# Kernel optimization log

Hardware: AMD Instinct MI355X
Metric: run time of the kernel (lower is better)

## Reference

```python
import jax, jax.numpy as jnp
import numpy as np

HIDDEN = 1024


def setup_inputs() -> dict:
    key = jax.random.key(0)
    ks = jax.random.split(key, 8)
    B, S, H = 64, 2048, HIDDEN
    scale = 1.0 / np.sqrt(H)
    return {
        "decoder_hidden": jax.random.normal(ks[0], (B, H), jnp.float32),
        "encoder_outputs": jax.random.normal(ks[1], (B, S, 2 * H), jnp.float32),
        "coverage": jax.random.uniform(ks[2], (B, S), jnp.float32),
        "mask": jnp.ones((B, S), jnp.int32),
        # parameters (nn.Linear weight layout: (out, in); we store transposed for x @ W)
        "W_h": jax.random.normal(ks[3], (2 * H, H), jnp.float32) * scale,
        "W_d": jax.random.normal(ks[4], (H, H), jnp.float32) * scale,
        "W_c": jax.random.normal(ks[5], (1, H), jnp.float32) * scale,
        "v": jax.random.normal(ks[6], (H, 1), jnp.float32) * scale,
    }


def reference(decoder_hidden, encoder_outputs, coverage, mask, W_h, W_d, W_c, v):
    # energy: (B, S, H) = tanh(enc@W_h + dec@W_d broadcast over S + coverage*W_c)
    enc_proj = jnp.einsum("bse,eh->bsh", encoder_outputs, W_h)
    dec_proj = (decoder_hidden @ W_d)[:, None, :]            # (B,1,H)
    cov_proj = coverage[:, :, None] * W_c[0][None, None, :]  # (B,S,H)
    energy = jnp.tanh(enc_proj + dec_proj + cov_proj)
    scores = jnp.einsum("bsh,h->bs", energy, v[:, 0])        # (B,S)
    scores = jnp.where(mask == 0, jnp.float32(-10000.0), scores)
    attn_weights = jax.nn.softmax(scores, axis=1)            # (B,S)
    coverage_new = coverage + attn_weights
    context = jnp.einsum("bs,bse->be", attn_weights, encoder_outputs)  # (B,2H)
    return (context, attn_weights, coverage_new)
```

## Files before the change

kernel.cpp:

```cpp
#include <hip/hip_runtime.h>
#include <hip/hip_bf16.h>
#include <stdint.h>

#define BATCH 64
#define SEQ   2048
#define HID   1024
#define EDIM  2048

#define BM 128
#define BN 512
#define BK 32
#define KSTEPS (EDIM / BK)
#define SMEM_BYTES (65536 + 16384 + 512 + 2048)

typedef __bf16 bf16x8 __attribute__((ext_vector_type(8)));
typedef float  f32x16 __attribute__((ext_vector_type(16)));
typedef float  f32x4v __attribute__((ext_vector_type(4)));

__device__ __forceinline__ unsigned short f2bf(float x) {
    __hip_bfloat16 h = __float2bfloat16(x);
    return __builtin_bit_cast(unsigned short, h);
}

__device__ __forceinline__ uint4 pack8(f32x4v f0, f32x4v f1) {
    uint4 r;
    r.x = (unsigned)f2bf(f0.x) | ((unsigned)f2bf(f0.y) << 16);
    r.y = (unsigned)f2bf(f0.z) | ((unsigned)f2bf(f0.w) << 16);
    r.z = (unsigned)f2bf(f1.x) | ((unsigned)f2bf(f1.y) << 16);
    r.w = (unsigned)f2bf(f1.z) | ((unsigned)f2bf(f1.w) << 16);
    return r;
}

__device__ __forceinline__ void gload16(const void* g, void* l) {
    __builtin_amdgcn_global_load_lds(
        (const __attribute__((address_space(1))) void*)g,
        (__attribute__((address_space(3))) void*)l, 16, 0, 0);
}

__device__ __forceinline__ f32x4v ntload4(const float* p) {
    return __builtin_nontemporal_load((const f32x4v*)p);
}

__device__ __forceinline__ int a_addr(int row, int g) {
    return ((row << 6) + (g << 4)) ^ ((row & 7) << 4);
}

__global__ void wh_transpose_kernel(const float* __restrict__ Wh,
                                    unsigned short* __restrict__ Wt) {
    __shared__ float tile[32][33];
    int bx = blockIdx.x & 63;
    int by = blockIdx.x >> 6;
    int e0 = bx * 32, h0 = by * 32;
    int tx = threadIdx.x & 31, ty = threadIdx.x >> 5;
    #pragma unroll
    for (int i = 0; i < 4; ++i)
        tile[ty + 8 * i][tx] = Wh[(size_t)(e0 + ty + 8 * i) * HID + h0 + tx];
    __syncthreads();
    if (ty < 4) {
        uint4 wv;
        unsigned short* ws = (unsigned short*)&wv;
        #pragma unroll
        for (int j = 0; j < 8; ++j) ws[j] = f2bf(tile[ty * 8 + j][tx]);
        int h = h0 + tx;
        *(uint4*)&Wt[(size_t)((e0 >> 3) + ty) * 8192 + (h >> 9) * 4096 + (h & 511) * 8] = wv;
    }
}

__global__ void dec_proj_kernel(const float* __restrict__ dec,
                                const float* __restrict__ Wd,
                                float* __restrict__ dp) {
    int gid = blockIdx.x * 256 + threadIdx.x;
    int b = gid >> 10, h = gid & 1023;
    const float* dr = dec + b * HID;
    float acc = 0.f;
    #pragma unroll 4
    for (int k = 0; k < HID; ++k) acc = fmaf(dr[k], Wd[(size_t)k * HID + h], acc);
    dp[gid] = acc;
}

__global__ __launch_bounds__(512, 2) void scores_kernel(
    const float* __restrict__ enc, const float* __restrict__ cov,
    const unsigned short* __restrict__ Wt, const float* __restrict__ dp,
    const float* __restrict__ Wc, const float* __restrict__ vv,
    float* __restrict__ spart_out)
{
    extern __shared__ char smem[];
    unsigned short* BlS  = (unsigned short*)smem;
    char*  AlB   = smem + 65536;
    float* cov_s = (float*)(smem + 81920);
    float* sred  = (float*)(smem + 82432);

    const int tid  = threadIdx.x;
    const int lane = tid & 63;
    const int wid  = tid >> 6;
    const int wm   = wid >> 2;
    const int wn   = wid & 3;
    const int l31  = lane & 31;
    const int hi   = lane >> 5;

    const int bid  = blockIdx.x;
    const int half = (bid & 7) >> 2;
    const int m    = ((bid >> 3) << 2) | (bid & 3);
    const int b    = m >> 4;
    const int s0   = (m & 15) * BM;

    const float* Abase = enc + (size_t)(b * SEQ + s0) * EDIM;

    const int arow = tid >> 2;
    const int ag   = tid & 3;

    f32x16 acc[2][4];
    #pragma unroll
    for (int mi = 0; mi < 2; ++mi)
        #pragma unroll
        for (int nj = 0; nj < 4; ++nj)
            #pragma unroll
            for (int r = 0; r < 16; ++r) acc[mi][nj][r] = 0.f;

    if (tid < BM) cov_s[tid] = cov[b * SEQ + s0 + tid];

    {
        const unsigned short* bsrc = Wt + half * 4096 + (size_t)tid * 8;
        unsigned short* bdst = BlS + tid * 8;
        #pragma unroll
        for (int j = 0; j < 4; ++j)
            gload16(bsrc + (size_t)j * 8192, bdst + j * 4096);
        const float* ap = Abase + (size_t)arow * EDIM + ag * 8;
        *(uint4*)(AlB + a_addr(arow, ag)) = pack8(ntload4(ap), ntload4(ap + 4));
    }
    __syncthreads();

    f32x4v a0n, a1n;
    for (int kk = 0; kk < KSTEPS; ++kk) {
        const int cur = kk & 1, nxt = cur ^ 1;
        const unsigned short* Bcur = BlS + cur * 16384;
        const char* Acur = AlB + cur * 8192;

        if (kk + 1 < KSTEPS) {
            const unsigned short* bsrc =
                Wt + (size_t)(kk + 1) * 32768 + half * 4096 + (size_t)tid * 8;
            unsigned short* bdst = BlS + nxt * 16384 + tid * 8;
            #pragma unroll
            for (int j = 0; j < 4; ++j)
                gload16(bsrc + (size_t)j * 8192, bdst + j * 4096);
            const float* ap = Abase + (size_t)arow * EDIM + (kk + 1) * BK + ag * 8;
            a0n = ntload4(ap);
            a1n = ntload4(ap + 4);
        }

        #pragma unroll
        for (int ks = 0; ks < 2; ++ks) {
            const int g = 2 * ks + hi;
            bf16x8 afr0 = *(const bf16x8*)(Acur + a_addr(wm * 64 + l31, g));
            bf16x8 afr1 = *(const bf16x8*)(Acur + a_addr(wm * 64 + 32 + l31, g));
            #pragma unroll
            for (int nj = 0; nj < 4; ++nj) {
                bf16x8 bfr = *(const bf16x8*)(Bcur +
                    (size_t)g * 4096 + (size_t)(wn * 128 + nj * 32 + l31) * 8);
                acc[0][nj] = __builtin_amdgcn_mfma_f32_32x32x16_bf16(
                    afr0, bfr, acc[0][nj], 0, 0, 0);
                acc[1][nj] = __builtin_amdgcn_mfma_f32_32x32x16_bf16(
                    afr1, bfr, acc[1][nj], 0, 0, 0);
            }
        }

        if (kk + 1 < KSTEPS)
            *(uint4*)(AlB + nxt * 8192 + a_addr(arow, ag)) = pack8(a0n, a1n);
        __syncthreads();
    }

    float dv[4], wcv[4], vvv[4];
    #pragma unroll
    for (int nj = 0; nj < 4; ++nj) {
        const int h = half * BN + wn * 128 + nj * 32 + l31;
        dv[nj]  = dp[b * HID + h];
        wcv[nj] = Wc[h];
        vvv[nj] = vv[h];
    }
    #pragma unroll
    for (int mi = 0; mi < 2; ++mi) {
        #pragma unroll
        for (int r = 0; r < 16; ++r) {
            const int row = wm * 64 + mi * 32 + (r & 3) + 8 * (r >> 2) + 4 * hi;
            const float cv = cov_s[row];
            float x = 0.f;
            #pragma unroll
            for (int nj = 0; nj < 4; ++nj) {
                float pre = acc[mi][nj][r] + dv[nj] + cv * wcv[nj];
                float pc = fminf(pre, 20.0f);
                float e2 = __expf(2.0f * pc);
                x = fmaf((e2 - 1.0f) / (e2 + 1.0f), vvv[nj], x);
            }
            x += __shfl_xor(x, 1);
            x += __shfl_xor(x, 2);
            x += __shfl_xor(x, 4);
            x += __shfl_xor(x, 8);
            x += __shfl_xor(x, 16);
            if (l31 == 0) sred[row * 4 + wn] = x;
        }
    }
    __syncthreads();
    if (tid < BM) {
        float s = sred[tid * 4] + sred[tid * 4 + 1] + sred[tid * 4 + 2] + sred[tid * 4 + 3];
        spart_out[(size_t)half * BATCH * SEQ + b * SEQ + s0 + tid] = s;
    }
}

__global__ void softmax_kernel(const float* __restrict__ spart,
                               const int* __restrict__ mask,
                               const float* __restrict__ cov,
                               float* __restrict__ out)
{
    __shared__ float red[8];
    int b = blockIdx.x, tid = threadIdx.x;
    float vals[8];
    float mx = -1e30f;
    #pragma unroll
    for (int i = 0; i < 8; ++i) {
        int s = tid + i * 256;
        float sc = spart[b * SEQ + s] + spart[BATCH * SEQ + b * SEQ + s];
        sc = (mask[b * SEQ + s] == 0) ? -10000.0f : sc;
        vals[i] = sc;
        mx = fmaxf(mx, sc);
    }
    for (int m = 1; m < 64; m <<= 1) mx = fmaxf(mx, __shfl_xor(mx, m));
    if ((tid & 63) == 0) red[tid >> 6] = mx;
    __syncthreads();
    mx = fmaxf(fmaxf(red[0], red[1]), fmaxf(red[2], red[3]));
    float sum = 0.f;
    #pragma unroll
    for (int i = 0; i < 8; ++i) { vals[i] = __expf(vals[i] - mx); sum += vals[i]; }
    for (int m = 1; m < 64; m <<= 1) sum += __shfl_xor(sum, m);
    if ((tid & 63) == 0) red[4 + (tid >> 6)] = sum;
    __syncthreads();
    sum = red[4] + red[5] + red[6] + red[7];
    float inv = 1.0f / sum;
    float* attn = out + BATCH * EDIM;
    float* covn = attn + BATCH * SEQ;
    #pragma unroll
    for (int i = 0; i < 8; ++i) {
        int s = tid + i * 256;
        float w = vals[i] * inv;
        attn[b * SEQ + s] = w;
        covn[b * SEQ + s] = cov[b * SEQ + s] + w;
    }
}

__global__ void context_kernel(const float* __restrict__ enc,
                               const float* __restrict__ attn,
                               float* __restrict__ ctx)
{
    __shared__ float w_s[SEQ];
    int b  = blockIdx.x >> 3;
    int e0 = (blockIdx.x & 7) * 256;
    int tid = threadIdx.x;
    for (int i = tid; i < SEQ; i += 256) w_s[i] = attn[b * SEQ + i];
    __syncthreads();
    const float* ep = enc + (size_t)b * SEQ * EDIM + e0 + tid;
    float acc = 0.f;
    #pragma unroll 8
    for (int s = 0; s < SEQ; ++s)
        acc = fmaf(w_s[s], __builtin_nontemporal_load(ep + (size_t)s * EDIM), acc);
    ctx[b * EDIM + e0 + tid] = acc;
}

extern "C" void kernel_launch(void* const* d_in, const int* in_sizes, int n_in,
                              void* d_out, int out_size, void* d_ws, size_t ws_size,
                              hipStream_t stream) {
    const float* dec  = (const float*)d_in[0];
    const float* enc  = (const float*)d_in[1];
    const float* cov  = (const float*)d_in[2];
    const int*   mask = (const int*)d_in[3];
    const float* Wh   = (const float*)d_in[4];
    const float* Wd   = (const float*)d_in[5];
    const float* Wc   = (const float*)d_in[6];
    const float* v    = (const float*)d_in[7];
    float* out = (float*)d_out;

    unsigned short* Wt = (unsigned short*)d_ws;
    float* dp    = (float*)((char*)d_ws + (size_t)HID * EDIM * 2);
    float* spart = dp + BATCH * HID;

    (void)hipFuncSetAttribute((const void*)scores_kernel,
                              hipFuncAttributeMaxDynamicSharedMemorySize, SMEM_BYTES);

    wh_transpose_kernel<<<dim3(64 * 32), dim3(256), 0, stream>>>(Wh, Wt);
    dec_proj_kernel<<<dim3(BATCH * HID / 256), dim3(256), 0, stream>>>(dec, Wd, dp);
    scores_kernel<<<dim3((SEQ * BATCH / BM) * 2), dim3(512), SMEM_BYTES, stream>>>(
        enc, cov, Wt, dp, Wc, v, spart);
    softmax_kernel<<<dim3(BATCH), dim3(256), 0, stream>>>(spart, mask, cov, out);
    context_kernel<<<dim3(BATCH * (EDIM / 256)), dim3(256), 0, stream>>>(enc, out + BATCH * EDIM, out);
}
```

Before: 1.141 ms.

## Deepen scores GEMM pipeline to four-stage LDS ring with prefetch distance two

The scores GEMM main loop moves from a double-buffered B tile with a one-step lookahead to a four-slot LDS ring for B, filled two K-steps ahead, with A held in two register stages. Plain __syncthreads is replaced by explicit s_waitcnt vmcnt/lgkmcnt counts and raw barriers, so only the oldest loads must land before each step. MFMA issue is split into two halves fenced by sched_barrier and raised with s_setprio, so LDS fragment reads overlap the first half of the math. This is meant to hide global-load latency and the stalls at each barrier. In exchange LDS grows to about 150KB per block, and correctness now depends on the hand-written wait counts matching the number of outstanding loads.

```diff
diff --git a/kernel.cpp b/kernel.cpp
--- a/kernel.cpp
+++ b/kernel.cpp
@@ -11,7 +11,7 @@
 #define BN 512
 #define BK 32
 #define KSTEPS (EDIM / BK)
-#define SMEM_BYTES (65536 + 16384 + 512 + 2048)
+#define SMEM_BYTES 150016
 
 typedef __bf16 bf16x8 __attribute__((ext_vector_type(8)));
 typedef float  f32x16 __attribute__((ext_vector_type(16)));
@@ -78,6 +78,8 @@
     dp[gid] = acc;
 }
 
+#define MFMA32(a, bfv, c) __builtin_amdgcn_mfma_f32_32x32x16_bf16(a, bfv, c, 0, 0, 0)
+
 __global__ __launch_bounds__(512, 2) void scores_kernel(
     const float* __restrict__ enc, const float* __restrict__ cov,
     const unsigned short* __restrict__ Wt, const float* __restrict__ dp,
@@ -85,10 +87,10 @@
     float* __restrict__ spart_out)
 {
     extern __shared__ char smem[];
-    unsigned short* BlS  = (unsigned short*)smem;
-    char*  AlB   = smem + 65536;
-    float* cov_s = (float*)(smem + 81920);
-    float* sred  = (float*)(smem + 82432);
+    unsigned short* BlS = (unsigned short*)smem;
+    char*  AlB   = smem + 131072;
+    float* cov_s = (float*)(smem + 147456);
+    float* sred  = (float*)(smem + 147968);
 
     const int tid  = threadIdx.x;
     const int lane = tid & 63;
@@ -105,9 +107,10 @@
     const int s0   = (m & 15) * BM;
 
     const float* Abase = enc + (size_t)(b * SEQ + s0) * EDIM;
-
     const int arow = tid >> 2;
     const int ag   = tid & 3;
+
+    const unsigned short* Bsrc0 = Wt + half * 4096 + (size_t)tid * 8;
 
     f32x16 acc[2][4];
     #pragma unroll
@@ -117,57 +120,87 @@
             #pragma unroll
             for (int r = 0; r < 16; ++r) acc[mi][nj][r] = 0.f;
 
+    f32x4v aL0[2], aL1[2];
+
+    {
+        const float* ap = Abase + (size_t)arow * EDIM + ag * 8;
+        aL0[0] = ntload4(ap); aL1[0] = ntload4(ap + 4);
+    }
+    #pragma unroll
+    for (int j = 0; j < 4; ++j)
+        gload16(Bsrc0 + (size_t)j * 8192, BlS + j * 4096 + tid * 8);
+    asm volatile("s_waitcnt vmcnt(4)" ::: "memory");
+    *(uint4*)(AlB + a_addr(arow, ag)) = pack8(aL0[0], aL1[0]);
+    {
+        const float* ap = Abase + (size_t)arow * EDIM + BK + ag * 8;
+        aL0[1] = ntload4(ap); aL1[1] = ntload4(ap + 4);
+    }
+    #pragma unroll
+    for (int j = 0; j < 4; ++j)
+        gload16(Bsrc0 + (size_t)(4 + j) * 8192, BlS + 16384 + j * 4096 + tid * 8);
+    asm volatile("s_waitcnt vmcnt(6) lgkmcnt(0)" ::: "memory");
+    __builtin_amdgcn_s_barrier();
+
+    for (int kk4 = 0; kk4 < KSTEPS; kk4 += 4) {
+        #pragma unroll
+        for (int u = 0; u < 4; ++u) {
+            const int kk = kk4 + u;
+            if (kk + 2 < KSTEPS) {
+                const float* ap = Abase + (size_t)arow * EDIM + (kk + 2) * BK + ag * 8;
+                aL0[u & 1] = ntload4(ap); aL1[u & 1] = ntload4(ap + 4);
+                const unsigned short* bs = Bsrc0 + (size_t)(kk + 2) * 32768;
+                unsigned short* bd = BlS + ((u + 2) & 3) * 16384 + tid * 8;
+                #pragma unroll
+                for (int j = 0; j < 4; ++j)
+                    gload16(bs + (size_t)j * 8192, bd + j * 4096);
+            }
+            const unsigned short* Bcur = BlS + u * 16384;
+            const char* Acur = AlB + (u & 1) * 8192;
+
+            bf16x8 afr[2][2], bfr[2][4];
+            #pragma unroll
+            for (int ks = 0; ks < 2; ++ks) {
+                const int g = 2 * ks + hi;
+                afr[ks][0] = *(const bf16x8*)(Acur + a_addr(wm * 64 + l31, g));
+                afr[ks][1] = *(const bf16x8*)(Acur + a_addr(wm * 64 + 32 + l31, g));
+                #pragma unroll
+                for (int nj = 0; nj < 4; ++nj)
+                    bfr[ks][nj] = *(const bf16x8*)(Bcur +
+                        (size_t)g * 4096 + (size_t)(wn * 128 + nj * 32 + l31) * 8);
+            }
+            asm volatile("s_waitcnt lgkmcnt(6)" ::: "memory");
+            __builtin_amdgcn_sched_barrier(0);
+            __builtin_amdgcn_s_setprio(1);
+            #pragma unroll
+            for (int nj = 0; nj < 4; ++nj) {
+                acc[0][nj] = MFMA32(afr[0][0], bfr[0][nj], acc[0][nj]);
+                acc[1][nj] = MFMA32(afr[0][1], bfr[0][nj], acc[1][nj]);
+            }
+            __builtin_amdgcn_s_setprio(0);
+            asm volatile("s_waitcnt lgkmcnt(0)" ::: "memory");
+            __builtin_amdgcn_sched_barrier(0);
+            __builtin_amdgcn_s_setprio(1);
+            #pragma unroll
+            for (int nj = 0; nj < 4; ++nj) {
+                acc[0][nj] = MFMA32(afr[1][0], bfr[1][nj], acc[0][nj]);
+                acc[1][nj] = MFMA32(afr[1][1], bfr[1][nj], acc[1][nj]);
+            }
+            __builtin_amdgcn_s_setprio(0);
+
+            if (kk + 1 < KSTEPS)
+                *(uint4*)(AlB + ((u + 1) & 1) * 8192 + a_addr(arow, ag)) =
+                    pack8(aL0[(u + 1) & 1], aL1[(u + 1) & 1]);
+
+            if (kk + 2 < KSTEPS)
+                asm volatile("s_waitcnt vmcnt(6) lgkmcnt(0)" ::: "memory");
+            else
+                asm volatile("s_waitcnt vmcnt(0) lgkmcnt(0)" ::: "memory");
+            __builtin_amdgcn_s_barrier();
+        }
+    }
+
     if (tid < BM) cov_s[tid] = cov[b * SEQ + s0 + tid];
-
-    {
-        const unsigned short* bsrc = Wt + half * 4096 + (size_t)tid * 8;
-        unsigned short* bdst = BlS + tid * 8;
-        #pragma unroll
-        for (int j = 0; j < 4; ++j)
-            gload16(bsrc + (size_t)j * 8192, bdst + j * 4096);
-        const float* ap = Abase + (size_t)arow * EDIM + ag * 8;
-        *(uint4*)(AlB + a_addr(arow, ag)) = pack8(ntload4(ap), ntload4(ap + 4));
-    }
-    __syncthreads();
-
-    f32x4v a0n, a1n;
-    for (int kk = 0; kk < KSTEPS; ++kk) {
-        const int cur = kk & 1, nxt = cur ^ 1;
-        const unsigned short* Bcur = BlS + cur * 16384;
-        const char* Acur = AlB + cur * 8192;
-
-        if (kk + 1 < KSTEPS) {
-            const unsigned short* bsrc =
-                Wt + (size_t)(kk + 1) * 32768 + half * 4096 + (size_t)tid * 8;
-            unsigned short* bdst = BlS + nxt * 16384 + tid * 8;
-            #pragma unroll
-            for (int j = 0; j < 4; ++j)
-                gload16(bsrc + (size_t)j * 8192, bdst + j * 4096);
-            const float* ap = Abase + (size_t)arow * EDIM + (kk + 1) * BK + ag * 8;
-            a0n = ntload4(ap);
-            a1n = ntload4(ap + 4);
-        }
-
-        #pragma unroll
-        for (int ks = 0; ks < 2; ++ks) {
-            const int g = 2 * ks + hi;
-            bf16x8 afr0 = *(const bf16x8*)(Acur + a_addr(wm * 64 + l31, g));
-            bf16x8 afr1 = *(const bf16x8*)(Acur + a_addr(wm * 64 + 32 + l31, g));
-            #pragma unroll
-            for (int nj = 0; nj < 4; ++nj) {
-                bf16x8 bfr = *(const bf16x8*)(Bcur +
-                    (size_t)g * 4096 + (size_t)(wn * 128 + nj * 32 + l31) * 8);
-                acc[0][nj] = __builtin_amdgcn_mfma_f32_32x32x16_bf16(
-                    afr0, bfr, acc[0][nj], 0, 0, 0);
-                acc[1][nj] = __builtin_amdgcn_mfma_f32_32x32x16_bf16(
-                    afr1, bfr, acc[1][nj], 0, 0, 0);
-            }
-        }
-
-        if (kk + 1 < KSTEPS)
-            *(uint4*)(AlB + nxt * 8192 + a_addr(arow, ag)) = pack8(a0n, a1n);
-        __syncthreads();
-    }
+    __syncthreads();
 
     float dv[4], wcv[4], vvv[4];
     #pragma unroll
```

Result: no change. 1.134 ms (-0.6%).

## Shrink score GEMM N-tile to 128 with 256-thread blocks and 8 partial splits

Applied to the files above, without the earlier changes.

Reshapes the scores GEMM tiling. BN drops from 512 to 128 and each block now has 4 waves (256 threads) instead of 8, with static shared memory sized for higher occupancy. The W_h transpose layout changes to match, and the softmax now sums 8 partial score planes instead of 2. Each encoder A tile is now read and converted to bf16 four times as often, since there are 8 N-splits instead of 2, and the nontemporal loads become plain loads. The aim is more resident blocks and better latency hiding, at the cost of much more global traffic on the large encoder tensor.

```diff
diff --git a/kernel.cpp b/kernel.cpp
--- a/kernel.cpp
+++ b/kernel.cpp
@@ -8,10 +8,10 @@
 #define EDIM  2048
 
 #define BM 128
-#define BN 512
+#define BN 128
 #define BK 32
 #define KSTEPS (EDIM / BK)
-#define SMEM_BYTES (65536 + 16384 + 512 + 2048)
+#define BS (BATCH * SEQ)
 
 typedef __bf16 bf16x8 __attribute__((ext_vector_type(8)));
 typedef float  f32x16 __attribute__((ext_vector_type(16)));
@@ -37,10 +37,6 @@
         (__attribute__((address_space(3))) void*)l, 16, 0, 0);
 }
 
-__device__ __forceinline__ f32x4v ntload4(const float* p) {
-    return __builtin_nontemporal_load((const f32x4v*)p);
-}
-
 __device__ __forceinline__ int a_addr(int row, int g) {
     return ((row << 6) + (g << 4)) ^ ((row & 7) << 4);
 }
@@ -62,7 +58,7 @@
         #pragma unroll
         for (int j = 0; j < 8; ++j) ws[j] = f2bf(tile[ty * 8 + j][tx]);
         int h = h0 + tx;
-        *(uint4*)&Wt[(size_t)((e0 >> 3) + ty) * 8192 + (h >> 9) * 4096 + (h & 511) * 8] = wv;
+        *(uint4*)&Wt[(size_t)((e0 >> 3) + ty) * 8192 + (h >> 7) * 1024 + (h & 127) * 8] = wv;
     }
 }
 
@@ -78,101 +74,104 @@
     dp[gid] = acc;
 }
 
-__global__ __launch_bounds__(512, 2) void scores_kernel(
+#define MFMA32(a, bfv, c) __builtin_amdgcn_mfma_f32_32x32x16_bf16(a, bfv, c, 0, 0, 0)
+
+__global__ __launch_bounds__(256, 4) void scores_kernel(
     const float* __restrict__ enc, const float* __restrict__ cov,
     const unsigned short* __restrict__ Wt, const float* __restrict__ dp,
     const float* __restrict__ Wc, const float* __restrict__ vv,
     float* __restrict__ spart_out)
 {
-    extern __shared__ char smem[];
-    unsigned short* BlS  = (unsigned short*)smem;
-    char*  AlB   = smem + 65536;
-    float* cov_s = (float*)(smem + 81920);
-    float* sred  = (float*)(smem + 82432);
+    __shared__ unsigned short Bl[2][4096];
+    __shared__ char Al[2][8192];
+    __shared__ float cov_s[BM];
+    __shared__ float sred[BM][2];
 
     const int tid  = threadIdx.x;
     const int lane = tid & 63;
-    const int wid  = tid >> 6;
-    const int wm   = wid >> 2;
-    const int wn   = wid & 3;
+    const int w    = tid >> 6;
+    const int wr   = w >> 1;
+    const int wc   = w & 1;
     const int l31  = lane & 31;
     const int hi   = lane >> 5;
 
-    const int bid  = blockIdx.x;
-    const int half = (bid & 7) >> 2;
-    const int m    = ((bid >> 3) << 2) | (bid & 3);
-    const int b    = m >> 4;
-    const int s0   = (m & 15) * BM;
+    const int bid    = blockIdx.x;
+    const int ns     = bid & 7;
+    const int mindex = bid >> 3;
+    const int b      = mindex >> 4;
+    const int s0     = (mindex & 15) * BM;
 
     const float* Abase = enc + (size_t)(b * SEQ + s0) * EDIM;
-
-    const int arow = tid >> 2;
-    const int ag   = tid & 3;
-
-    f32x16 acc[2][4];
+    const int arow = tid >> 1;
+    const int agb  = (tid & 1) * 2;
+
+    const unsigned short* Bw = Wt + (size_t)w * 8192 + ns * 1024 + (size_t)lane * 8;
+
+    f32x16 acc[2][2];
     #pragma unroll
     for (int mi = 0; mi < 2; ++mi)
         #pragma unroll
-        for (int nj = 0; nj < 4; ++nj)
+        for (int nj = 0; nj < 2; ++nj)
             #pragma unroll
             for (int r = 0; r < 16; ++r) acc[mi][nj][r] = 0.f;
 
     if (tid < BM) cov_s[tid] = cov[b * SEQ + s0 + tid];
 
     {
-        const unsigned short* bsrc = Wt + half * 4096 + (size_t)tid * 8;
-        unsigned short* bdst = BlS + tid * 8;
-        #pragma unroll
-        for (int j = 0; j < 4; ++j)
-            gload16(bsrc + (size_t)j * 8192, bdst + j * 4096);
-        const float* ap = Abase + (size_t)arow * EDIM + ag * 8;
-        *(uint4*)(AlB + a_addr(arow, ag)) = pack8(ntload4(ap), ntload4(ap + 4));
-    }
-    __syncthreads();
-
-    f32x4v a0n, a1n;
+        gload16(Bw,       &Bl[0][w * 1024 + lane * 8]);
+        gload16(Bw + 512, &Bl[0][w * 1024 + 512 + lane * 8]);
+        #pragma unroll
+        for (int j = 0; j < 2; ++j) {
+            const int g = agb + j;
+            const float* ap = Abase + (size_t)arow * EDIM + g * 8;
+            f32x4v f0 = *(const f32x4v*)ap;
+            f32x4v f1 = *(const f32x4v*)(ap + 4);
+            *(uint4*)&Al[0][a_addr(arow, g)] = pack8(f0, f1);
+        }
+    }
+    __syncthreads();
+
     for (int kk = 0; kk < KSTEPS; ++kk) {
         const int cur = kk & 1, nxt = cur ^ 1;
-        const unsigned short* Bcur = BlS + cur * 16384;
-        const char* Acur = AlB + cur * 8192;
+        f32x4v a00, a01, a10, a11;
 
         if (kk + 1 < KSTEPS) {
-            const unsigned short* bsrc =
-                Wt + (size_t)(kk + 1) * 32768 + half * 4096 + (size_t)tid * 8;
-            unsigned short* bdst = BlS + nxt * 16384 + tid * 8;
-            #pragma unroll
-            for (int j = 0; j < 4; ++j)
-                gload16(bsrc + (size_t)j * 8192, bdst + j * 4096);
-            const float* ap = Abase + (size_t)arow * EDIM + (kk + 1) * BK + ag * 8;
-            a0n = ntload4(ap);
-            a1n = ntload4(ap + 4);
+            const unsigned short* bs = Bw + (size_t)(kk + 1) * 32768;
+            gload16(bs,       &Bl[nxt][w * 1024 + lane * 8]);
+            gload16(bs + 512, &Bl[nxt][w * 1024 + 512 + lane * 8]);
+            const float* ap = Abase + (size_t)arow * EDIM + (kk + 1) * BK + agb * 8;
+            a00 = *(const f32x4v*)ap;       a01 = *(const f32x4v*)(ap + 4);
+            a10 = *(const f32x4v*)(ap + 8); a11 = *(const f32x4v*)(ap + 12);
         }
 
         #pragma unroll
         for (int ks = 0; ks < 2; ++ks) {
             const int g = 2 * ks + hi;
-            bf16x8 afr0 = *(const bf16x8*)(Acur + a_addr(wm * 64 + l31, g));
-            bf16x8 afr1 = *(const bf16x8*)(Acur + a_addr(wm * 64 + 32 + l31, g));
-            #pragma unroll
-            for (int nj = 0; nj < 4; ++nj) {
-                bf16x8 bfr = *(const bf16x8*)(Bcur +
-                    (size_t)g * 4096 + (size_t)(wn * 128 + nj * 32 + l31) * 8);
-                acc[0][nj] = __builtin_amdgcn_mfma_f32_32x32x16_bf16(
-                    afr0, bfr, acc[0][nj], 0, 0, 0);
-                acc[1][nj] = __builtin_amdgcn_mfma_f32_32x32x16_bf16(
-                    afr1, bfr, acc[1][nj], 0, 0, 0);
-            }
-        }
-
-        if (kk + 1 < KSTEPS)
-            *(uint4*)(AlB + nxt * 8192 + a_addr(arow, ag)) = pack8(a0n, a1n);
+            bf16x8 afr[2], bfr[2];
+            #pragma unroll
+            for (int mi = 0; mi < 2; ++mi)
+                afr[mi] = *(const bf16x8*)(&Al[cur][a_addr(wr * 64 + mi * 32 + l31, g)]);
+            #pragma unroll
+            for (int nj = 0; nj < 2; ++nj)
+                bfr[nj] = *(const bf16x8*)(&Bl[cur][g * 1024 + (wc * 64 + nj * 32 + l31) * 8]);
+            #pragma unroll
+            for (int mi = 0; mi < 2; ++mi)
+                #pragma unroll
+                for (int nj = 0; nj < 2; ++nj)
+                    acc[mi][nj] = MFMA32(afr[mi], bfr[nj], acc[mi][nj]);
+        }
+
+        if (kk + 1 < KSTEPS) {
+            *(uint4*)&Al[nxt][a_addr(arow, agb)]     = pack8(a00, a01);
+            *(uint4*)&Al[nxt][a_addr(arow, agb + 1)] = pack8(a10, a11);
+        }
         __syncthreads();
     }
 
-    float dv[4], wcv[4], vvv[4];
-    #pragma unroll
-    for (int nj = 0; nj < 4; ++nj) {
-        const int h = half * BN + wn * 128 + nj * 32 + l31;
+    float dv[2], wcv[2], vvv[2];
+    #pragma unroll
+    for (int nj = 0; nj < 2; ++nj) {
+        const int h = ns * BN + wc * 64 + nj * 32 + l31;
         dv[nj]  = dp[b * HID + h];
         wcv[nj] = Wc[h];
         vvv[nj] = vv[h];
@@ -181,11 +180,11 @@
     for (int mi = 0; mi < 2; ++mi) {
         #pragma unroll
         for (int r = 0; r < 16; ++r) {
-            const int row = wm * 64 + mi * 32 + (r & 3) + 8 * (r >> 2) + 4 * hi;
+            const int row = wr * 64 + mi * 32 + (r & 3) + 8 * (r >> 2) + 4 * hi;
             const float cv = cov_s[row];
             float x = 0.f;
             #pragma unroll
-            for (int nj = 0; nj < 4; ++nj) {
+            for (int nj = 0; nj < 2; ++nj) {
                 float pre = acc[mi][nj][r] + dv[nj] + cv * wcv[nj];
                 float pc = fminf(pre, 20.0f);
                 float e2 = __expf(2.0f * pc);
@@ -196,14 +195,12 @@
             x += __shfl_xor(x, 4);
             x += __shfl_xor(x, 8);
             x += __shfl_xor(x, 16);
-            if (l31 == 0) sred[row * 4 + wn] = x;
-        }
-    }
-    __syncthreads();
-    if (tid < BM) {
-        float s = sred[tid * 4] + sred[tid * 4 + 1] + sred[tid * 4 + 2] + sred[tid * 4 + 3];
-        spart_out[(size_t)half * BATCH * SEQ + b * SEQ + s0 + tid] = s;
-    }
+            if (l31 == 0) sred[row][wc] = x;
+        }
+    }
+    __syncthreads();
+    if (tid < BM)
+        spart_out[(size_t)ns * BS + b * SEQ + s0 + tid] = sred[tid][0] + sred[tid][1];
 }
 
 __global__ void softmax_kernel(const float* __restrict__ spart,
@@ -218,7 +215,9 @@
     #pragma unroll
     for (int i = 0; i < 8; ++i) {
         int s = tid + i * 256;
-        float sc = spart[b * SEQ + s] + spart[BATCH * SEQ + b * SEQ + s];
+        float sc = 0.f;
+        #pragma unroll
+        for (int k = 0; k < 8; ++k) sc += spart[(size_t)k * BS + b * SEQ + s];
         sc = (mask[b * SEQ + s] == 0) ? -10000.0f : sc;
         vals[i] = sc;
         mx = fmaxf(mx, sc);
@@ -281,12 +280,9 @@
     float* dp    = (float*)((char*)d_ws + (size_t)HID * EDIM * 2);
     float* spart = dp + BATCH * HID;
 
-    (void)hipFuncSetAttribute((const void*)scores_kernel,
-                              hipFuncAttributeMaxDynamicSharedMemorySize, SMEM_BYTES);
-
     wh_transpose_kernel<<<dim3(64 * 32), dim3(256), 0, stream>>>(Wh, Wt);
     dec_proj_kernel<<<dim3(BATCH * HID / 256), dim3(256), 0, stream>>>(dec, Wd, dp);
-    scores_kernel<<<dim3((SEQ * BATCH / BM) * 2), dim3(512), SMEM_BYTES, stream>>>(
+    scores_kernel<<<dim3((SEQ * BATCH / BM) * 8), dim3(256), 0, stream>>>(
         enc, cov, Wt, dp, Wc, v, spart);
     softmax_kernel<<<dim3(BATCH), dim3(256), 0, stream>>>(spart, mask, cov, out);
     context_kernel<<<dim3(BATCH * (EDIM / 256)), dim3(256), 0, stream>>>(enc, out + BATCH * EDIM, out);
```

New measurement: 1.469 ms. +28.8%, slower.
